# Kernel optimization log

Measured on AMD Instinct MI355X. Metric: run time of the kernel, lower is better.

## Reference

```python
import jax, jax.numpy as jnp
import numpy as np

N, D, H, C, K, L = 50000, 256, 128, 40, 4, 2
E = 800000


def setup_inputs() -> dict:
    key = jax.random.key(0)
    ks = jax.random.split(key, 20)
    g = lambda k, s: jax.random.normal(k, s, dtype=jnp.float32) * 0.05
    z = lambda s: jnp.zeros(s, dtype=jnp.float32)
    return {
        "x": jax.random.normal(ks[0], (N, D), dtype=jnp.float32),
        "edge_index": jax.random.randint(ks[1], (2, E), 0, N, dtype=jnp.int32),
        "fc0_w": g(ks[2], (D, H)), "fc0_b": z((H,)),
        "fc1_w": g(ks[3], (H, C)), "fc1_b": z((C,)),
        "env_w": g(ks[4], (L, H, K)), "env_b": z((L, K)),
        "conv_w": g(ks[5], (L, K, 2 * H, H)),
        "q_w": g(ks[6], (H, H)), "q_b": z((H,)),
        "k_w": g(ks[7], (H, H)), "k_b": z((H,)),
        "v_w": g(ks[8], (H, H)), "v_b": z((H,)),
        "envp_w": g(ks[9], (H, K)), "envp_b": z((K,)),
        "genv_w": g(ks[10], (K, H, H)),
        "gt_w": g(ks[11], (H, H)), "gt_b": z((H,)),
    }


def _gcn_conv(h, row, col, n):
    # symmetric normalization using in-degree array (deg computed from col, as in source)
    deg = jax.ops.segment_sum(jnp.ones_like(col, dtype=h.dtype), col, num_segments=n)
    inv = jnp.where(deg > 0, 1.0 / jnp.sqrt(deg), 0.0)
    val = inv[col] * inv[row]                      # [E]
    msg = val[:, None] * h[row]                    # [E, H] gather
    return jax.ops.segment_sum(msg, col, num_segments=n)  # scatter to dst


def _canet_conv(h, row, col, env, w):
    # sum_k e_k [W_D^k * A_norm h ; W_S^k * h] via cat + per-env GEMM, residual
    hi = jnp.concatenate([_gcn_conv(h, row, col, h.shape[0]), h], axis=1)  # [N, 2H]
    out_k = jnp.einsum('nd,kdh->nkh', hi, w)       # [N, K, H]
    return jnp.einsum('nk,nkh->nh', env, out_k) + h


def _linear_transformer(h, q_w, q_b, k_w, k_b, v_w, v_b, envp_w, envp_b):
    n = h.shape[0]
    q = h @ q_w + q_b
    k = h @ k_w + k_b
    v = h @ v_w + v_b
    q = q / jnp.maximum(jnp.linalg.norm(q), 1e-12)  # fro-norm of whole matrix
    k = k / jnp.maximum(jnp.linalg.norm(k), 1e-12)
    ksum = jnp.sum(k, axis=0)                       # k^T @ ones -> [H]
    attn_norm = 1.0 + (q @ ksum)[:, None] / n       # [N,1]
    gr = (v + q @ (k.T @ v) / n) / jnp.maximum(attn_norm, 1e-12)
    return gr, gr @ envp_w + envp_b


def _forward(x, edge_index, fc0_w, fc0_b, fc1_w, fc1_b, env_w, env_b, conv_w,
             q_w, q_b, k_w, k_b, v_w, v_b, envp_w, envp_b, genv_w, gt_w, gt_b):
    row, col = edge_index[0], edge_index[1]
    h = jax.nn.relu(x @ fc0_w + fc0_b)
    for i in range(L):
        logits = h @ env_w[i] + env_b[i]            # node env encoder
        env = jax.nn.softmax(logits, axis=-1)       # eval-mode sampling
        h = jax.nn.relu(_canet_conv(h, row, col, env, conv_w[i]))
    local_logits = h @ fc1_w + fc1_b                # [N, C]
    gr, glog = _linear_transformer(h, q_w, q_b, k_w, k_b, v_w, v_b, envp_w, envp_b)
    genv = jax.nn.softmax(glog, axis=-1)            # [N, K]
    gpe = jnp.einsum('nh,khe->nke', gr, genv_w)     # per-env global transforms
    ctx = jnp.einsum('nk,nkh->nh', genv, gpe)
    gh = jax.nn.relu(ctx @ gt_w + gt_b)
    global_logits = gh @ fc1_w + fc1_b
    return 0.5 * (local_logits + global_logits)     # fused prediction


def reference(x, edge_index, fc0_w, fc0_b, fc1_w, fc1_b, env_w, env_b, conv_w,
              q_w, q_b, k_w, k_b, v_w, v_b, envp_w, envp_b, genv_w, gt_w, gt_b):
    return _forward(x, edge_index, fc0_w, fc0_b, fc1_w, fc1_b, env_w, env_b, conv_w,
                    q_w, q_b, k_w, k_b, v_w, v_b, envp_w, envp_b, genv_w, gt_w, gt_b)
```

## Files before the change

### kernel.cpp

```cpp
#include <hip/hip_runtime.h>

#define DEV __device__ __forceinline__

static constexpr int NN = 50000;
static constexpr int DD = 256;
static constexpr int HH = 128;
static constexpr int CC = 40;
static constexpr int KK = 4;
static constexpr int EE = 800000;
static constexpr int MP = 50176;
static constexpr int SKV = 196;
static constexpr int CPB = 8;
static constexpr int CSB = 391;
static constexpr int MBC = 391;

typedef __attribute__((ext_vector_type(8))) short bf16x8;
typedef __attribute__((ext_vector_type(4))) float f32x4;

DEV unsigned short f2bf(float f) {
  union { float f; unsigned int i; } c; c.f = f;
  unsigned int x = c.i;
  x += 0x7FFFu + ((x >> 16) & 1u);
  return (unsigned short)(x >> 16);
}
DEV float bfbits2f(unsigned int hi16bits) {
  union { unsigned int i; float f; } c; c.i = hi16bits; return c.f;
}

__global__ void MLEI_12970801234193_kernel(float* out, int n) {
  int i = blockIdx.x * blockDim.x + threadIdx.x;
  if (i < n) out[i] = 7.0f;
}

__global__ void zero_i32_kernel(int* p, int n) {
  int i = blockIdx.x * blockDim.x + threadIdx.x;
  if (i < n) p[i] = 0;
}

__global__ void padzero_kernel(unsigned short* kT, unsigned short* vT) {
  int i = blockIdx.x * blockDim.x + threadIdx.x;
  const int PW = MP - NN;
  if (i >= HH * PW) return;
  int f = i / PW, c = i - f * PW;
  kT[(size_t)f * MP + NN + c] = 0;
  vT[(size_t)f * MP + NN + c] = 0;
}

__global__ void tcvt_kernel(const float* __restrict__ src, unsigned short* __restrict__ dst,
                            int K, int N, int nm) {
  int i = blockIdx.x * blockDim.x + threadIdx.x;
  int tot = nm * K * N;
  if (i >= tot) return;
  int m = i / (K * N);
  int rem = i - m * K * N;
  int k = rem / N;
  int n = rem - k * N;
  dst[(size_t)m * K * N + (size_t)n * K + k] = f2bf(src[i]);
}

__global__ __launch_bounds__(256) void mgemm_kernel(
    const float* __restrict__ A, const float* __restrict__ Aadd, int lda,
    const unsigned short* __restrict__ Bt, int K,
    int emode, float* __restrict__ out, int ldo,
    const float* __restrict__ bias, const float* __restrict__ resid, int ldr,
    const float* __restrict__ anorm, const float* __restrict__ red,
    unsigned short* __restrict__ outT,
    unsigned short* __restrict__ outBf, const float* __restrict__ rowscale,
    int M, int Nd) {
  __shared__ unsigned short As[2][128][40];
  __shared__ unsigned short Bs[2][128][40];
  const int tid = threadIdx.x, lane = tid & 63, wave = tid >> 6;
  const int quad = lane >> 4, l16 = lane & 15;
  const int wm = (wave >> 1) * 64, wn = (wave & 1) * 64;
  const int bm = blockIdx.x * 128;
  const int srow = tid >> 1, skh = (tid & 1) * 16;
  const int grow = bm + srow;
  const bool rowok = grow < M;
  const bool colok = srow < Nd;
  const int NCH = K >> 5;

  f32x4 acc[4][4];
#pragma unroll
  for (int i = 0; i < 4; ++i)
#pragma unroll
    for (int j = 0; j < 4; ++j)
#pragma unroll
      for (int r = 0; r < 4; ++r) acc[i][j][r] = 0.f;

  float vaA[16], vaB[16];
  bf16x8 bA0, bA1, bB0, bB1;

  auto LOAD = [&](int kc, float (&va)[16], bf16x8& b0, bf16x8& b1) {
    int k0 = kc << 5;
    if (rowok) {
      const float* ap = A + (size_t)grow * lda + k0 + skh;
      float4 v0 = *(const float4*)(ap + 0), v1 = *(const float4*)(ap + 4);
      float4 v2 = *(const float4*)(ap + 8), v3 = *(const float4*)(ap + 12);
      va[0] = v0.x; va[1] = v0.y; va[2] = v0.z; va[3] = v0.w;
      va[4] = v1.x; va[5] = v1.y; va[6] = v1.z; va[7] = v1.w;
      va[8] = v2.x; va[9] = v2.y; va[10] = v2.z; va[11] = v2.w;
      va[12] = v3.x; va[13] = v3.y; va[14] = v3.z; va[15] = v3.w;
      if (Aadd) {
        const float* ap2 = Aadd + (size_t)grow * lda + k0 + skh;
        float4 w0 = *(const float4*)(ap2 + 0), w1 = *(const float4*)(ap2 + 4);
        float4 w2 = *(const float4*)(ap2 + 8), w3 = *(const float4*)(ap2 + 12);
        va[0] += w0.x; va[1] += w0.y; va[2] += w0.z; va[3] += w0.w;
        va[4] += w1.x; va[5] += w1.y; va[6] += w1.z; va[7] += w1.w;
        va[8] += w2.x; va[9] += w2.y; va[10] += w2.z; va[11] += w2.w;
        va[12] += w3.x; va[13] += w3.y; va[14] += w3.z; va[15] += w3.w;
      }
    }
    if (colok) {
      const unsigned short* bp = Bt + (size_t)srow * K + k0 + skh;
      b0 = *(const bf16x8*)(bp);
      b1 = *(const bf16x8*)(bp + 8);
    } else {
#pragma unroll
      for (int z = 0; z < 8; ++z) { b0[z] = 0; b1[z] = 0; }
    }
  };

  auto STORE = [&](int buf, const float (&va)[16], const bf16x8& b0, const bf16x8& b1) {
    bf16x8 p0, p1;
    if (rowok) {
#pragma unroll
      for (int z = 0; z < 8; ++z) { p0[z] = (short)f2bf(va[z]); p1[z] = (short)f2bf(va[z + 8]); }
    } else {
#pragma unroll
      for (int z = 0; z < 8; ++z) { p0[z] = 0; p1[z] = 0; }
    }
    *(bf16x8*)&As[buf][srow][skh] = p0;
    *(bf16x8*)&As[buf][srow][skh + 8] = p1;
    *(bf16x8*)&Bs[buf][srow][skh] = b0;
    *(bf16x8*)&Bs[buf][srow][skh + 8] = b1;
  };

  auto MFMA = [&](int buf) {
    bf16x8 af[4], bfr[4];
#pragma unroll
    for (int i = 0; i < 4; ++i) af[i] = *(const bf16x8*)&As[buf][wm + i * 16 + l16][quad * 8];
#pragma unroll
    for (int j = 0; j < 4; ++j) bfr[j] = *(const bf16x8*)&Bs[buf][wn + j * 16 + l16][quad * 8];
#pragma unroll
    for (int i = 0; i < 4; ++i)
#pragma unroll
      for (int j = 0; j < 4; ++j)
        acc[i][j] = __builtin_amdgcn_mfma_f32_16x16x32_bf16(af[i], bfr[j], acc[i][j], 0, 0, 0);
  };

  LOAD(0, vaA, bA0, bA1);
  if (NCH > 1) LOAD(1, vaB, bB0, bB1);
  STORE(0, vaA, bA0, bA1);
  __syncthreads();

  for (int kc = 0; kc < NCH; kc += 2) {
    if (kc + 2 < NCH) LOAD(kc + 2, vaA, bA0, bA1);
    MFMA(0);
    if (kc + 1 < NCH) STORE(1, vaB, bB0, bB1);
    __syncthreads();
    if (kc + 1 < NCH) {
      if (kc + 3 < NCH) LOAD(kc + 3, vaB, bB0, bB1);
      MFMA(1);
      if (kc + 2 < NCH) STORE(0, vaA, bA0, bA1);
      __syncthreads();
    }
  }

  float s2 = (emode == 3) ? red[2] : 0.f;
#pragma unroll
  for (int j = 0; j < 4; ++j) {
    int col = wn + j * 16 + l16;
    if (col >= Nd) continue;
    float bv = bias ? bias[col] : 0.f;
#pragma unroll
    for (int i = 0; i < 4; ++i) {
      int row0 = bm + wm + i * 16 + quad * 4;
      if (row0 >= M) continue;
      float o[4];
#pragma unroll
      for (int r = 0; r < 4; ++r) {
        float a = acc[i][j][r];
        int row = row0 + r;
        if (emode == 0) o[r] = a + bv;
        else if (emode == 1) o[r] = fmaxf(a + bv, 0.f);
        else if (emode == 3) o[r] = (resid[(size_t)row * ldr + col] + a * s2) / anorm[row];
        else o[r] = 0.5f * a + bv;
        out[(size_t)row * ldo + col] = o[r];
      }
      if (outT) {
        ushort4 pk;
        pk.x = f2bf(o[0]); pk.y = f2bf(o[1]); pk.z = f2bf(o[2]); pk.w = f2bf(o[3]);
        *(ushort4*)&outT[(size_t)col * MP + row0] = pk;
      }
      if (outBf) {
#pragma unroll
        for (int r = 0; r < 4; ++r) {
          float rs = rowscale ? rowscale[row0 + r] : 1.f;
          outBf[(size_t)(row0 + r) * 128 + col] = f2bf(o[r] * rs);
        }
      }
    }
  }
}

__global__ __launch_bounds__(256) void mgemm_qkv_kernel(
    const float* __restrict__ A,
    const unsigned short* __restrict__ Btq, const unsigned short* __restrict__ Btk,
    const unsigned short* __restrict__ Btv,
    const float* __restrict__ q_b, const float* __restrict__ k_b,
    const float* __restrict__ v_b,
    float* __restrict__ outq, float* __restrict__ outk, float* __restrict__ outv,
    unsigned short* __restrict__ kT, unsigned short* __restrict__ vT, int M) {
  __shared__ unsigned short As[2][128][40];
  __shared__ unsigned short Bs[2][128][40];
  const int which = blockIdx.x % 3;
  const int bx = blockIdx.x / 3;
  const unsigned short* Bt = (which == 0) ? Btq : (which == 1) ? Btk : Btv;
  const float* bias = (which == 0) ? q_b : (which == 1) ? k_b : v_b;
  float* out = (which == 0) ? outq : (which == 1) ? outk : outv;
  unsigned short* outT = (which == 0) ? nullptr : (which == 1) ? kT : vT;

  const int tid = threadIdx.x, lane = tid & 63, wave = tid >> 6;
  const int quad = lane >> 4, l16 = lane & 15;
  const int wm = (wave >> 1) * 64, wn = (wave & 1) * 64;
  const int bm = bx * 128;
  const int srow = tid >> 1, skh = (tid & 1) * 16;
  const int grow = bm + srow;
  const bool rowok = grow < M;
  const int NCH = 4;

  f32x4 acc[4][4];
#pragma unroll
  for (int i = 0; i < 4; ++i)
#pragma unroll
    for (int j = 0; j < 4; ++j)
#pragma unroll
      for (int r = 0; r < 4; ++r) acc[i][j][r] = 0.f;

  float vaA[16], vaB[16];
  bf16x8 bA0, bA1, bB0, bB1;

  auto LOAD = [&](int kc, float (&va)[16], bf16x8& b0, bf16x8& b1) {
    int k0 = kc << 5;
    if (rowok) {
      const float* ap = A + (size_t)grow * 128 + k0 + skh;
      float4 v0 = *(const float4*)(ap + 0), v1 = *(const float4*)(ap + 4);
      float4 v2 = *(const float4*)(ap + 8), v3 = *(const float4*)(ap + 12);
      va[0] = v0.x; va[1] = v0.y; va[2] = v0.z; va[3] = v0.w;
      va[4] = v1.x; va[5] = v1.y; va[6] = v1.z; va[7] = v1.w;
      va[8] = v2.x; va[9] = v2.y; va[10] = v2.z; va[11] = v2.w;
      va[12] = v3.x; va[13] = v3.y; va[14] = v3.z; va[15] = v3.w;
    }
    const unsigned short* bp = Bt + (size_t)srow * 128 + k0 + skh;
    b0 = *(const bf16x8*)(bp);
    b1 = *(const bf16x8*)(bp + 8);
  };

  auto STORE = [&](int buf, const float (&va)[16], const bf16x8& b0, const bf16x8& b1) {
    bf16x8 p0, p1;
    if (rowok) {
#pragma unroll
      for (int z = 0; z < 8; ++z) { p0[z] = (short)f2bf(va[z]); p1[z] = (short)f2bf(va[z + 8]); }
    } else {
#pragma unroll
      for (int z = 0; z < 8; ++z) { p0[z] = 0; p1[z] = 0; }
    }
    *(bf16x8*)&As[buf][srow][skh] = p0;
    *(bf16x8*)&As[buf][srow][skh + 8] = p1;
    *(bf16x8*)&Bs[buf][srow][skh] = b0;
    *(bf16x8*)&Bs[buf][srow][skh + 8] = b1;
  };

  auto MFMA = [&](int buf) {
    bf16x8 af[4], bfr[4];
#pragma unroll
    for (int i = 0; i < 4; ++i) af[i] = *(const bf16x8*)&As[buf][wm + i * 16 + l16][quad * 8];
#pragma unroll
    for (int j = 0; j < 4; ++j) bfr[j] = *(const bf16x8*)&Bs[buf][wn + j * 16 + l16][quad * 8];
#pragma unroll
    for (int i = 0; i < 4; ++i)
#pragma unroll
      for (int j = 0; j < 4; ++j)
        acc[i][j] = __builtin_amdgcn_mfma_f32_16x16x32_bf16(af[i], bfr[j], acc[i][j], 0, 0, 0);
  };

  LOAD(0, vaA, bA0, bA1);
  LOAD(1, vaB, bB0, bB1);
  STORE(0, vaA, bA0, bA1);
  __syncthreads();

  for (int kc = 0; kc < NCH; kc += 2) {
    if (kc + 2 < NCH) LOAD(kc + 2, vaA, bA0, bA1);
    MFMA(0);
    if (kc + 1 < NCH) STORE(1, vaB, bB0, bB1);
    __syncthreads();
    if (kc + 1 < NCH) {
      if (kc + 3 < NCH) LOAD(kc + 3, vaB, bB0, bB1);
      MFMA(1);
      if (kc + 2 < NCH) STORE(0, vaA, bA0, bA1);
      __syncthreads();
    }
  }

#pragma unroll
  for (int j = 0; j < 4; ++j) {
    int col = wn + j * 16 + l16;
    float bv = bias[col];
#pragma unroll
    for (int i = 0; i < 4; ++i) {
      int row0 = bm + wm + i * 16 + quad * 4;
      if (row0 >= M) continue;
      float o[4];
#pragma unroll
      for (int r = 0; r < 4; ++r) {
        o[r] = acc[i][j][r] + bv;
        out[(size_t)(row0 + r) * 128 + col] = o[r];
      }
      if (outT) {
        ushort4 pk;
        pk.x = f2bf(o[0]); pk.y = f2bf(o[1]); pk.z = f2bf(o[2]); pk.w = f2bf(o[3]);
        *(ushort4*)&outT[(size_t)col * MP + row0] = pk;
      }
    }
  }
}

__global__ __launch_bounds__(256) void ktv_mfma_kernel(
    const unsigned short* __restrict__ kT, const unsigned short* __restrict__ vT,
    float* __restrict__ part) {
  __shared__ unsigned short As[2][128][40];
  __shared__ unsigned short Bs[2][128][40];
  const int tid = threadIdx.x, lane = tid & 63, wave = tid >> 6;
  const int quad = lane >> 4, l16 = lane & 15;
  const int wm = (wave >> 1) * 64, wn = (wave & 1) * 64;
  const int srow = tid >> 1, skh = (tid & 1) * 16;

  f32x4 acc[4][4];
#pragma unroll
  for (int i = 0; i < 4; ++i)
#pragma unroll
    for (int j = 0; j < 4; ++j)
#pragma unroll
      for (int r = 0; r < 4; ++r) acc[i][j][r] = 0.f;

  const int nb0 = blockIdx.x * (CPB * 32);
  bf16x8 kA0, kA1, vA0, vA1, kB0, kB1, vB0, vB1;

  auto LOAD = [&](int c, bf16x8& k0, bf16x8& k1, bf16x8& v0, bf16x8& v1) {
    int nb = nb0 + c * 32;
    const unsigned short* kp = kT + (size_t)srow * MP + nb + skh;
    k0 = *(const bf16x8*)(kp);
    k1 = *(const bf16x8*)(kp + 8);
    const unsigned short* vp = vT + (size_t)srow * MP + nb + skh;
    v0 = *(const bf16x8*)(vp);
    v1 = *(const bf16x8*)(vp + 8);
  };
  auto STORE = [&](int buf, const bf16x8& k0, const bf16x8& k1, const bf16x8& v0, const bf16x8& v1) {
    *(bf16x8*)&As[buf][srow][skh] = k0;
    *(bf16x8*)&As[buf][srow][skh + 8] = k1;
    *(bf16x8*)&Bs[buf][srow][skh] = v0;
    *(bf16x8*)&Bs[buf][srow][skh + 8] = v1;
  };
  auto MFMA = [&](int buf) {
    bf16x8 af[4], bfr[4];
#pragma unroll
    for (int i = 0; i < 4; ++i) af[i] = *(const bf16x8*)&As[buf][wm + i * 16 + l16][quad * 8];
#pragma unroll
    for (int j = 0; j < 4; ++j) bfr[j] = *(const bf16x8*)&Bs[buf][wn + j * 16 + l16][quad * 8];
#pragma unroll
    for (int i = 0; i < 4; ++i)
#pragma unroll
      for (int j = 0; j < 4; ++j)
        acc[i][j] = __builtin_amdgcn_mfma_f32_16x16x32_bf16(af[i], bfr[j], acc[i][j], 0, 0, 0);
  };

  LOAD(0, kA0, kA1, vA0, vA1);
  LOAD(1, kB0, kB1, vB0, vB1);
  STORE(0, kA0, kA1, vA0, vA1);
  __syncthreads();

  for (int c = 0; c < CPB; c += 2) {
    if (c + 2 < CPB) LOAD(c + 2, kA0, kA1, vA0, vA1);
    MFMA(0);
    if (c + 1 < CPB) STORE(1, kB0, kB1, vB0, vB1);
    __syncthreads();
    if (c + 1 < CPB) {
      if (c + 3 < CPB) LOAD(c + 3, kB0, kB1, vB0, vB1);
      MFMA(1);
      if (c + 2 < CPB) STORE(0, kA0, kA1, vA0, vA1);
      __syncthreads();
    }
  }

  float* pb = part + (size_t)blockIdx.x * 16384;
#pragma unroll
  for (int j = 0; j < 4; ++j) {
    int col = wn + j * 16 + l16;
#pragma unroll
    for (int i = 0; i < 4; ++i) {
      int row0 = wm + i * 16 + quad * 4;
      *(f32x4*)&pb[col * 128 + row0] = acc[i][j];
    }
  }
}

__global__ void ktv_reduce_kernel(const float* __restrict__ part,
                                  unsigned short* __restrict__ Btktv) {
  int i = blockIdx.x * blockDim.x + threadIdx.x;
  if (i >= 16384) return;
  float s0 = 0.f, s1 = 0.f, s2 = 0.f, s3 = 0.f;
  int b = 0;
  for (; b + 3 < SKV; b += 4) {
    s0 += part[(size_t)b * 16384 + i];
    s1 += part[(size_t)(b + 1) * 16384 + i];
    s2 += part[(size_t)(b + 2) * 16384 + i];
    s3 += part[(size_t)(b + 3) * 16384 + i];
  }
  for (; b < SKV; ++b) s0 += part[(size_t)b * 16384 + i];
  Btktv[i] = f2bf((s0 + s1) + (s2 + s3));
}

__global__ __launch_bounds__(256) void mconv_kernel(
    const float* __restrict__ A1, const float* __restrict__ A2,
    const float* __restrict__ env, const unsigned short* __restrict__ Btc, int Kpe,
    int relu_resid, const float* __restrict__ resid, float* __restrict__ out,
    unsigned short* __restrict__ outBf, const float* __restrict__ rowscale, int M) {
  __shared__ unsigned short As[2][128][40];
  __shared__ unsigned short Bs[2][128][40];
  const int tid = threadIdx.x, lane = tid & 63, wave = tid >> 6;
  const int quad = lane >> 4, l16 = lane & 15;
  const int wm = (wave >> 1) * 64, wn = (wave & 1) * 64;
  const int bm = blockIdx.x * 128;
  const int srow = tid >> 1, skh = (tid & 1) * 16;
  const int grow = bm + srow;
  const bool rowok = grow < M;

  float ev0 = 0.f, ev1 = 0.f, ev2 = 0.f, ev3 = 0.f;
  if (rowok) {
    float4 e4 = *(const float4*)&env[(size_t)grow * 4];
    ev0 = e4.x; ev1 = e4.y; ev2 = e4.z; ev3 = e4.w;
  }

  const int npe = Kpe >> 5;
  const int NPH = npe << 2;

  f32x4 acc[4][4];
#pragma unroll
  for (int i = 0; i < 4; ++i)
#pragma unroll
    for (int j = 0; j < 4; ++j)
#pragma unroll
      for (int r = 0; r < 4; ++r) acc[i][j][r] = 0.f;

  float aC[16], aN[16];
  bf16x8 b0, b1;

  auto LOADA = [&](int kc, float (&dst)[16]) {
    int kof = kc << 5;
    const float* Asrc = A1;
    int ks = kof;
    if (A2 && kof >= 128) { Asrc = A2; ks = kof - 128; }
    if (rowok) {
      const float* ap = Asrc + (size_t)grow * 128 + ks + skh;
      float4 v0 = *(const float4*)(ap + 0), v1 = *(const float4*)(ap + 4);
      float4 v2 = *(const float4*)(ap + 8), v3 = *(const float4*)(ap + 12);
      dst[0] = v0.x; dst[1] = v0.y; dst[2] = v0.z; dst[3] = v0.w;
      dst[4] = v1.x; dst[5] = v1.y; dst[6] = v1.z; dst[7] = v1.w;
      dst[8] = v2.x; dst[9] = v2.y; dst[10] = v2.z; dst[11] = v2.w;
      dst[12] = v3.x; dst[13] = v3.y; dst[14] = v3.z; dst[15] = v3.w;
    }
  };

  auto LOADB = [&](int e, int kc) {
    const unsigned short* bp = Btc + ((size_t)e * 128 + srow) * Kpe + (kc << 5) + skh;
    b0 = *(const bf16x8*)(bp);
    b1 = *(const bf16x8*)(bp + 8);
  };

  auto STORE = [&](int buf, const float (&a)[16], float ev) {
    bf16x8 p0, p1;
    if (rowok) {
#pragma unroll
      for (int z = 0; z < 8; ++z) {
        p0[z] = (short)f2bf(a[z] * ev);
        p1[z] = (short)f2bf(a[z + 8] * ev);
      }
    } else {
#pragma unroll
      for (int z = 0; z < 8; ++z) { p0[z] = 0; p1[z] = 0; }
    }
    *(bf16x8*)&As[buf][srow][skh] = p0;
    *(bf16x8*)&As[buf][srow][skh + 8] = p1;
    *(bf16x8*)&Bs[buf][srow][skh] = b0;
    *(bf16x8*)&Bs[buf][srow][skh + 8] = b1;
  };

  auto MFMA = [&](int buf) {
    bf16x8 af[4], bfr[4];
#pragma unroll
    for (int i = 0; i < 4; ++i) af[i] = *(const bf16x8*)&As[buf][wm + i * 16 + l16][quad * 8];
#pragma unroll
    for (int j = 0; j < 4; ++j) bfr[j] = *(const bf16x8*)&Bs[buf][wn + j * 16 + l16][quad * 8];
#pragma unroll
    for (int i = 0; i < 4; ++i)
#pragma unroll
      for (int j = 0; j < 4; ++j)
        acc[i][j] = __builtin_amdgcn_mfma_f32_16x16x32_bf16(af[i], bfr[j], acc[i][j], 0, 0, 0);
  };

  LOADA(0, aC);
  LOADB(0, 0);
  if (npe > 1) LOADA(1, aN);
  STORE(0, aC, ev0);
  __syncthreads();

  for (int kc = 0; kc < npe; ++kc) {
#pragma unroll
    for (int e = 0; e < 4; ++e) {
      const int p = (kc << 2) + e;
      const int cur = e & 1;
      const bool more = (p + 1) < NPH;
      if (more) {
        LOADB((e + 1) & 3, kc + (e == 3 ? 1 : 0));
      }
      MFMA(cur);
      if (more) {
        if (e == 3) {
#pragma unroll
          for (int z = 0; z < 16; ++z) aC[z] = aN[z];
        }
        float evn = (e == 0) ? ev1 : (e == 1) ? ev2 : (e == 2) ? ev3 : ev0;
        STORE(cur ^ 1, aC, evn);
        if (e == 3 && kc + 2 < npe) LOADA(kc + 2, aN);
      }
      __syncthreads();
    }
  }

#pragma unroll
  for (int j = 0; j < 4; ++j) {
    int col = wn + j * 16 + l16;
#pragma unroll
    for (int i = 0; i < 4; ++i) {
      int row0 = bm + wm + i * 16 + quad * 4;
      if (row0 >= M) continue;
#pragma unroll
      for (int r = 0; r < 4; ++r) {
        int row = row0 + r;
        float a = acc[i][j][r];
        float o = relu_resid ? fmaxf(a + resid[(size_t)row * 128 + col], 0.f) : a;
        out[(size_t)row * 128 + col] = o;
        if (outBf) {
          float rs = rowscale ? rowscale[row] : 1.f;
          outBf[(size_t)row * 128 + col] = f2bf(o * rs);
        }
      }
    }
  }
}

__global__ void count_kernel(const int* ei, int* deg, int E) {
  int e = blockIdx.x * blockDim.x + threadIdx.x;
  if (e >= E) return;
  atomicAdd(&deg[ei[E + e]], 1);
}

__global__ __launch_bounds__(128) void scan1_kernel(const int* __restrict__ deg,
                                                    int* __restrict__ bsum, int n) {
  __shared__ int sh[128];
  int t = threadIdx.x;
  int i = blockIdx.x * 128 + t;
  sh[t] = (i < n) ? deg[i] : 0;
  __syncthreads();
  for (int off = 64; off > 0; off >>= 1) {
    if (t < off) sh[t] += sh[t + off];
    __syncthreads();
  }
  if (t == 0) bsum[blockIdx.x] = sh[0];
}

__global__ __launch_bounds__(512) void scan2_kernel(const int* __restrict__ bsum,
                                                    int* __restrict__ boff, int nb,
                                                    int* __restrict__ startN) {
  __shared__ int sh[512];
  int t = threadIdx.x;
  int v0 = (t < nb) ? bsum[t] : 0;
  sh[t] = v0;
  __syncthreads();
  for (int off = 1; off < 512; off <<= 1) {
    int v = sh[t];
    int add = (t >= off) ? sh[t - off] : 0;
    __syncthreads();
    sh[t] = v + add;
    __syncthreads();
  }
  if (t < nb) boff[t] = sh[t] - v0;
  if (t == nb - 1) *startN = sh[t];
}

__global__ __launch_bounds__(128) void scan3_kernel(const int* __restrict__ deg,
                                                    const int* __restrict__ boff,
                                                    int* __restrict__ start,
                                                    int* __restrict__ cursor,
                                                    float* __restrict__ inv, int n) {
  __shared__ int sh[128];
  int t = threadIdx.x;
  int i = blockIdx.x * 128 + t;
  int d = (i < n) ? deg[i] : 0;
  sh[t] = d;
  __syncthreads();
  for (int off = 1; off < 128; off <<= 1) {
    int v = sh[t];
    int add = (t >= off) ? sh[t - off] : 0;
    __syncthreads();
    sh[t] = v + add;
    __syncthreads();
  }
  if (i < n) {
    int p = boff[blockIdx.x] + sh[t] - d;
    start[i] = p; cursor[i] = p;
    inv[i] = (d > 0) ? rsqrtf((float)d) : 0.f;
  }
}

__global__ void fill_kernel(const int* ei, int* cursor, int* bucket, int E) {
  int e = blockIdx.x * blockDim.x + threadIdx.x;
  if (e >= E) return;
  int r = ei[e], c = ei[E + e];
  int pos = atomicAdd(&cursor[c], 1);
  bucket[pos] = r;
}

__global__ __launch_bounds__(256) void gather_kernel(
    const unsigned short* __restrict__ hs, const int* __restrict__ start,
    const int* __restrict__ bucket, const float* __restrict__ inv,
    float* __restrict__ agg, int n) {
  int node = blockIdx.x * 4 + (threadIdx.x >> 6);
  if (node >= n) return;
  const int lane = threadIdx.x & 63;
  const int half = lane >> 5, l32 = lane & 31;
  const int f4 = l32 * 4;
  int s0 = start[node], s1 = start[node + 1];
  float a0 = 0.f, a1 = 0.f, a2 = 0.f, a3 = 0.f;
  int j = s0 + half;
  for (; j + 2 < s1; j += 4) {
    int r0 = bucket[j], r1 = bucket[j + 2];
    uint2 u0 = *(const uint2*)&hs[(size_t)r0 * 128 + f4];
    uint2 u1 = *(const uint2*)&hs[(size_t)r1 * 128 + f4];
    a0 += bfbits2f(u0.x << 16); a1 += bfbits2f(u0.x & 0xFFFF0000u);
    a2 += bfbits2f(u0.y << 16); a3 += bfbits2f(u0.y & 0xFFFF0000u);
    a0 += bfbits2f(u1.x << 16); a1 += bfbits2f(u1.x & 0xFFFF0000u);
    a2 += bfbits2f(u1.y << 16); a3 += bfbits2f(u1.y & 0xFFFF0000u);
  }
  for (; j < s1; j += 2) {
    int r = bucket[j];
    uint2 u = *(const uint2*)&hs[(size_t)r * 128 + f4];
    a0 += bfbits2f(u.x << 16); a1 += bfbits2f(u.x & 0xFFFF0000u);
    a2 += bfbits2f(u.y << 16); a3 += bfbits2f(u.y & 0xFFFF0000u);
  }
  a0 += __shfl_xor(a0, 32);
  a1 += __shfl_xor(a1, 32);
  a2 += __shfl_xor(a2, 32);
  a3 += __shfl_xor(a3, 32);
  if (half == 0) {
    float iv = inv[node];
    *(float4*)&agg[(size_t)node * 128 + f4] = make_float4(iv * a0, iv * a1, iv * a2, iv * a3);
  }
}

__global__ __launch_bounds__(256) void env_softmax_kernel(const float* __restrict__ h,
                                                          const float* __restrict__ w,
                                                          const float* __restrict__ b,
                                                          float* __restrict__ env, int M) {
  __shared__ float hsd[64][129];
  __shared__ float ws[HH * KK];
  int tid = threadIdx.x;
  int base = blockIdx.x * 64;
  for (int i = tid; i < HH * KK; i += 256) ws[i] = w[i];
  {
    int row = tid >> 2, q4 = (tid & 3) * 32;
    int g = base + row;
    if (g < M) {
      const float* hp = h + (size_t)g * HH + q4;
#pragma unroll
      for (int z = 0; z < 8; ++z) {
        float4 v = *(const float4*)(hp + z * 4);
        hsd[row][q4 + z * 4 + 0] = v.x; hsd[row][q4 + z * 4 + 1] = v.y;
        hsd[row][q4 + z * 4 + 2] = v.z; hsd[row][q4 + z * 4 + 3] = v.w;
      }
    }
  }
  __syncthreads();
  if (tid < 64 && base + tid < M) {
    float l0 = b[0], l1 = b[1], l2 = b[2], l3 = b[3];
    for (int d = 0; d < HH; ++d) {
      float hv = hsd[tid][d];
      l0 += hv * ws[d * 4 + 0]; l1 += hv * ws[d * 4 + 1];
      l2 += hv * ws[d * 4 + 2]; l3 += hv * ws[d * 4 + 3];
    }
    float m = fmaxf(fmaxf(l0, l1), fmaxf(l2, l3));
    float e0 = __expf(l0 - m), e1 = __expf(l1 - m), e2 = __expf(l2 - m), e3 = __expf(l3 - m);
    float s = 1.f / (e0 + e1 + e2 + e3);
    *(float4*)(env + (size_t)(base + tid) * KK) = make_float4(e0 * s, e1 * s, e2 * s, e3 * s);
  }
}

__global__ __launch_bounds__(256) void colstats1_kernel(
    const float* __restrict__ q, const float* __restrict__ k,
    float* __restrict__ partK, float* __restrict__ partS, int n) {
  int tid = threadIdx.x, ty = tid >> 7, tx = tid & 127;
  int lo = blockIdx.x * 128 + ty, hi = min(n, blockIdx.x * 128 + 128);
  float ks = 0.f, sq = 0.f, sk = 0.f;
  for (int r = lo; r < hi; r += 2) {
    float kv = k[(size_t)r * HH + tx];
    float qv = q[(size_t)r * HH + tx];
    ks += kv; sq += qv * qv; sk += kv * kv;
  }
  __shared__ float sks[2][128];
  __shared__ float ssq[256], ssk[256];
  sks[ty][tx] = ks; ssq[tid] = sq; ssk[tid] = sk;
  __syncthreads();
  if (ty == 0) partK[(size_t)blockIdx.x * 128 + tx] = sks[0][tx] + sks[1][tx];
  for (int off = 128; off > 0; off >>= 1) {
    if (tid < off) { ssq[tid] += ssq[tid + off]; ssk[tid] += ssk[tid + off]; }
    __syncthreads();
  }
  if (tid == 0) { partS[blockIdx.x * 2] = ssq[0]; partS[blockIdx.x * 2 + 1] = ssk[0]; }
}

__global__ __launch_bounds__(256) void colstats2_kernel(
    const float* __restrict__ partK, const float* __restrict__ partS,
    float* __restrict__ ksum, float* __restrict__ red) {
  int t = threadIdx.x;
  if (t < 128) {
    float s = 0.f;
    for (int b = 0; b < CSB; ++b) s += partK[(size_t)b * 128 + t];
    ksum[t] = s;
  } else if (t == 128 || t == 129) {
    float s = 0.f;
    for (int b = 0; b < CSB; ++b) s += partS[b * 2 + (t - 128)];
    red[t - 128] = s;
  }
}

__global__ void scale_kernel(float* red, int n) {
  float nq = fmaxf(sqrtf(red[0]), 1e-12f);
  float nk = fmaxf(sqrtf(red[1]), 1e-12f);
  red[2] = 1.f / (nq * nk * (float)n);
}

__global__ __launch_bounds__(256) void anorm_kernel(const float* q, const float* ksum,
                                                    const float* red, float* anorm, int M) {
  __shared__ float ks[HH];
  for (int i = threadIdx.x; i < HH; i += blockDim.x) ks[i] = ksum[i];
  __syncthreads();
  int n = blockIdx.x * blockDim.x + threadIdx.x;
  if (n >= M) return;
  const float* qp = q + (size_t)n * HH;
  float d = 0.f;
  for (int i = 0; i < HH; ++i) d += qp[i] * ks[i];
  float a = 1.f + d * red[2];
  anorm[n] = fmaxf(a, 1e-12f);
}

extern "C" void kernel_launch(void* const* d_in, const int* in_sizes, int n_in,
                              void* d_out, int out_size, void* d_ws, size_t ws_size,
                              hipStream_t stream) {
  const float* x = (const float*)d_in[0];
  const int* ei = (const int*)d_in[1];
  const float* fc0_w = (const float*)d_in[2];
  const float* fc0_b = (const float*)d_in[3];
  const float* fc1_w = (const float*)d_in[4];
  const float* fc1_b = (const float*)d_in[5];
  const float* env_w = (const float*)d_in[6];
  const float* env_b = (const float*)d_in[7];
  const float* conv_w = (const float*)d_in[8];
  const float* q_w = (const float*)d_in[9];
  const float* q_b = (const float*)d_in[10];
  const float* k_w = (const float*)d_in[11];
  const float* k_b = (const float*)d_in[12];
  const float* v_w = (const float*)d_in[13];
  const float* v_b = (const float*)d_in[14];
  const float* envp_w = (const float*)d_in[15];
  const float* envp_b = (const float*)d_in[16];
  const float* genv_w = (const float*)d_in[17];
  const float* gt_w = (const float*)d_in[18];
  const float* gt_b = (const float*)d_in[19];
  float* out = (float*)d_out;

  const size_t NH = (size_t)NN * HH;
  float* W = (float*)d_ws;
  float* hA = W;
  float* hB = W + NH;
  float* agg = W + 2 * NH;
  float* vbuf = W + 3 * NH;
  float* gr = W + 4 * NH;
  float* env = W + 5 * NH;
  float* genv = env + (size_t)NN * KK;
  float* inv = genv + (size_t)NN * KK;
  float* anorm = inv + NN;
  float* ksum = anorm + NN;
  float* red = ksum + HH;
  int* deg = (int*)(red + 4);
  int* start = deg + NN;
  int* cursor = start + NN + 1;
  int* bucket = cursor + NN;
  int* bsum = bucket + EE;
  int* boff = bsum + CSB;
  unsigned short* wb = (unsigned short*)(((uintptr_t)(boff + CSB) + 15) & ~(uintptr_t)15);
  unsigned short* Btfc0 = wb;
  unsigned short* Btq = Btfc0 + 32768;
  unsigned short* Btk = Btq + 16384;
  unsigned short* Btv = Btk + 16384;
  unsigned short* Btgt = Btv + 16384;
  unsigned short* Btfc1 = Btgt + 16384;
  unsigned short* Btconv = Btfc1 + 5120;
  unsigned short* Btgenv = Btconv + 262144;
  unsigned short* Btktv = Btgenv + 65536;
  unsigned short* kTbf = Btktv + 16384;
  unsigned short* vTbf = kTbf + (size_t)HH * MP;
  unsigned short* hsb = vTbf + (size_t)HH * MP;
  float* part = (float*)(((uintptr_t)(hsb + NH) + 15) & ~(uintptr_t)15);
  float* partK = part + (size_t)SKV * 16384;
  float* partS = partK + (size_t)CSB * 128;

  float* q = agg;
  float* kb = hB;
  float* ctx = hB;
  float* gh = vbuf;

  dim3 b256(256);
  const int MB = MBC;

  zero_i32_kernel<<<dim3((NN + 255) / 256), b256, 0, stream>>>(deg, NN);
  padzero_kernel<<<dim3((HH * (MP - NN) + 255) / 256), b256, 0, stream>>>(kTbf, vTbf);

  count_kernel<<<dim3((EE + 255) / 256), b256, 0, stream>>>(ei, deg, EE);
  scan1_kernel<<<dim3(CSB), dim3(128), 0, stream>>>(deg, bsum, NN);
  scan2_kernel<<<dim3(1), dim3(512), 0, stream>>>(bsum, boff, CSB, start + NN);
  scan3_kernel<<<dim3(CSB), dim3(128), 0, stream>>>(deg, boff, start, cursor, inv, NN);
  fill_kernel<<<dim3((EE + 255) / 256), b256, 0, stream>>>(ei, cursor, bucket, EE);

  tcvt_kernel<<<dim3((32768 + 255) / 256), b256, 0, stream>>>(fc0_w, Btfc0, 256, 128, 1);
  tcvt_kernel<<<dim3((16384 + 255) / 256), b256, 0, stream>>>(q_w, Btq, 128, 128, 1);
  tcvt_kernel<<<dim3((16384 + 255) / 256), b256, 0, stream>>>(k_w, Btk, 128, 128, 1);
  tcvt_kernel<<<dim3((16384 + 255) / 256), b256, 0, stream>>>(v_w, Btv, 128, 128, 1);
  tcvt_kernel<<<dim3((16384 + 255) / 256), b256, 0, stream>>>(gt_w, Btgt, 128, 128, 1);
  tcvt_kernel<<<dim3((5120 + 255) / 256), b256, 0, stream>>>(fc1_w, Btfc1, 128, 40, 1);
  tcvt_kernel<<<dim3((262144 + 255) / 256), b256, 0, stream>>>(conv_w, Btconv, 256, 128, 8);
  tcvt_kernel<<<dim3((65536 + 255) / 256), b256, 0, stream>>>(genv_w, Btgenv, 128, 128, 4);

  mgemm_kernel<<<dim3(MB), b256, 0, stream>>>(
      x, nullptr, DD, Btfc0, 256, 1, hA, HH, fc0_b, nullptr, 0, nullptr, nullptr,
      nullptr, hsb, inv, NN, HH);

  float* hcur = hA;
  float* hnext = hB;
  for (int l = 0; l < 2; ++l) {
    env_softmax_kernel<<<dim3((NN + 63) / 64), b256, 0, stream>>>(
        hcur, env_w + (size_t)l * HH * KK, env_b + (size_t)l * KK, env, NN);
    gather_kernel<<<dim3(NN / 4), b256, 0, stream>>>(hsb, start, bucket, inv, agg, NN);
    mconv_kernel<<<dim3(MB), b256, 0, stream>>>(
        agg, hcur, env, Btconv + (size_t)l * 131072, 256, 1, hcur, hnext,
        (l == 0) ? hsb : nullptr, inv, NN);
    float* t = hcur; hcur = hnext; hnext = t;
  }

  mgemm_qkv_kernel<<<dim3(3 * MB), b256, 0, stream>>>(
      hcur, Btq, Btk, Btv, q_b, k_b, v_b, q, kb, vbuf, kTbf, vTbf, NN);

  colstats1_kernel<<<dim3(CSB), b256, 0, stream>>>(q, kb, partK, partS, NN);
  colstats2_kernel<<<dim3(1), b256, 0, stream>>>(partK, partS, ksum, red);
  ktv_mfma_kernel<<<dim3(SKV), b256, 0, stream>>>(kTbf, vTbf, part);
  ktv_reduce_kernel<<<dim3(64), b256, 0, stream>>>(part, Btktv);
  scale_kernel<<<dim3(1), dim3(1), 0, stream>>>(red, NN);
  anorm_kernel<<<dim3((NN + 255) / 256), b256, 0, stream>>>(q, ksum, red, anorm, NN);

  mgemm_kernel<<<dim3(MB), b256, 0, stream>>>(
      q, nullptr, HH, Btktv, 128, 3, gr, HH, nullptr, vbuf, HH, anorm, red,
      nullptr, nullptr, nullptr, NN, HH);

  env_softmax_kernel<<<dim3((NN + 63) / 64), b256, 0, stream>>>(gr, envp_w, envp_b, genv, NN);

  mconv_kernel<<<dim3(MB), b256, 0, stream>>>(
      gr, nullptr, genv, Btgenv, 128, 0, nullptr, ctx, nullptr, nullptr, NN);

  mgemm_kernel<<<dim3(MB), b256, 0, stream>>>(
      ctx, nullptr, HH, Btgt, 128, 1, gh, HH, gt_b, nullptr, 0, nullptr, nullptr,
      nullptr, nullptr, nullptr, NN, HH);

  mgemm_kernel<<<dim3(MB), b256, 0, stream>>>(
      hcur, gh, HH, Btfc1, 128, 5, out, CC, fc1_b, nullptr, 0, nullptr, nullptr,
      nullptr, nullptr, nullptr, NN, CC);
}
```

Before: 697.9 us.

## Fuse prep kernels, merge env softmax into gather, co-launch colstats with KtV

```diff
diff --git a/kernel.cpp b/kernel.cpp
--- a/kernel.cpp
+++ b/kernel.cpp
@@ -32,30 +32,51 @@
   if (i < n) out[i] = 7.0f;
 }
 
-__global__ void zero_i32_kernel(int* p, int n) {
-  int i = blockIdx.x * blockDim.x + threadIdx.x;
-  if (i < n) p[i] = 0;
-}
-
-__global__ void padzero_kernel(unsigned short* kT, unsigned short* vT) {
-  int i = blockIdx.x * blockDim.x + threadIdx.x;
-  const int PW = MP - NN;
-  if (i >= HH * PW) return;
-  int f = i / PW, c = i - f * PW;
-  kT[(size_t)f * MP + NN + c] = 0;
-  vT[(size_t)f * MP + NN + c] = 0;
-}
-
-__global__ void tcvt_kernel(const float* __restrict__ src, unsigned short* __restrict__ dst,
-                            int K, int N, int nm) {
-  int i = blockIdx.x * blockDim.x + threadIdx.x;
-  int tot = nm * K * N;
-  if (i >= tot) return;
+DEV void tc(const float* __restrict__ src, unsigned short* __restrict__ dst,
+            int i, int K, int N) {
   int m = i / (K * N);
   int rem = i - m * K * N;
   int k = rem / N;
   int n = rem - k * N;
   dst[(size_t)m * K * N + (size_t)n * K + k] = f2bf(src[i]);
+}
+
+__global__ __launch_bounds__(256) void prep_kernel(
+    int* __restrict__ deg, unsigned short* __restrict__ kT, unsigned short* __restrict__ vT,
+    const float* __restrict__ fc0_w, unsigned short* __restrict__ Btfc0,
+    const float* __restrict__ q_w, unsigned short* __restrict__ Btq,
+    const float* __restrict__ k_w, unsigned short* __restrict__ Btk,
+    const float* __restrict__ v_w, unsigned short* __restrict__ Btv,
+    const float* __restrict__ gt_w, unsigned short* __restrict__ Btgt,
+    const float* __restrict__ fc1_w, unsigned short* __restrict__ Btfc1,
+    const float* __restrict__ conv_w, unsigned short* __restrict__ Btconv,
+    const float* __restrict__ genv_w, unsigned short* __restrict__ Btgenv) {
+  int i = blockIdx.x * 256 + threadIdx.x;
+  if (i < NN) { deg[i] = 0; return; }
+  i -= NN;
+  const int PW = MP - NN;
+  if (i < HH * PW) {
+    int f = i / PW, c = i - f * PW;
+    kT[(size_t)f * MP + NN + c] = 0;
+    vT[(size_t)f * MP + NN + c] = 0;
+    return;
+  }
+  i -= HH * PW;
+  if (i < 32768) { tc(fc0_w, Btfc0, i, 256, 128); return; }
+  i -= 32768;
+  if (i < 16384) { tc(q_w, Btq, i, 128, 128); return; }
+  i -= 16384;
+  if (i < 16384) { tc(k_w, Btk, i, 128, 128); return; }
+  i -= 16384;
+  if (i < 16384) { tc(v_w, Btv, i, 128, 128); return; }
+  i -= 16384;
+  if (i < 16384) { tc(gt_w, Btgt, i, 128, 128); return; }
+  i -= 16384;
+  if (i < 5120) { tc(fc1_w, Btfc1, i, 128, 40); return; }
+  i -= 5120;
+  if (i < 262144) { tc(conv_w, Btconv, i, 256, 128); return; }
+  i -= 262144;
+  if (i < 65536) { tc(genv_w, Btgenv, i, 128, 128); }
 }
 
 __global__ __launch_bounds__(256) void mgemm_kernel(
@@ -325,82 +346,109 @@
   }
 }
 
-__global__ __launch_bounds__(256) void ktv_mfma_kernel(
+__global__ __launch_bounds__(256) void colstats_ktv_kernel(
     const unsigned short* __restrict__ kT, const unsigned short* __restrict__ vT,
-    float* __restrict__ part) {
+    float* __restrict__ part,
+    const float* __restrict__ q, const float* __restrict__ k,
+    float* __restrict__ partK, float* __restrict__ partS, int n) {
   __shared__ unsigned short As[2][128][40];
   __shared__ unsigned short Bs[2][128][40];
-  const int tid = threadIdx.x, lane = tid & 63, wave = tid >> 6;
-  const int quad = lane >> 4, l16 = lane & 15;
-  const int wm = (wave >> 1) * 64, wn = (wave & 1) * 64;
-  const int srow = tid >> 1, skh = (tid & 1) * 16;
-
-  f32x4 acc[4][4];
-#pragma unroll
-  for (int i = 0; i < 4; ++i)
-#pragma unroll
-    for (int j = 0; j < 4; ++j)
-#pragma unroll
-      for (int r = 0; r < 4; ++r) acc[i][j][r] = 0.f;
-
-  const int nb0 = blockIdx.x * (CPB * 32);
-  bf16x8 kA0, kA1, vA0, vA1, kB0, kB1, vB0, vB1;
-
-  auto LOAD = [&](int c, bf16x8& k0, bf16x8& k1, bf16x8& v0, bf16x8& v1) {
-    int nb = nb0 + c * 32;
-    const unsigned short* kp = kT + (size_t)srow * MP + nb + skh;
-    k0 = *(const bf16x8*)(kp);
-    k1 = *(const bf16x8*)(kp + 8);
-    const unsigned short* vp = vT + (size_t)srow * MP + nb + skh;
-    v0 = *(const bf16x8*)(vp);
-    v1 = *(const bf16x8*)(vp + 8);
-  };
-  auto STORE = [&](int buf, const bf16x8& k0, const bf16x8& k1, const bf16x8& v0, const bf16x8& v1) {
-    *(bf16x8*)&As[buf][srow][skh] = k0;
-    *(bf16x8*)&As[buf][srow][skh + 8] = k1;
-    *(bf16x8*)&Bs[buf][srow][skh] = v0;
-    *(bf16x8*)&Bs[buf][srow][skh + 8] = v1;
-  };
-  auto MFMA = [&](int buf) {
-    bf16x8 af[4], bfr[4];
-#pragma unroll
-    for (int i = 0; i < 4; ++i) af[i] = *(const bf16x8*)&As[buf][wm + i * 16 + l16][quad * 8];
-#pragma unroll
-    for (int j = 0; j < 4; ++j) bfr[j] = *(const bf16x8*)&Bs[buf][wn + j * 16 + l16][quad * 8];
+  const int tid = threadIdx.x;
+
+  if (blockIdx.x < SKV) {
+    const int lane = tid & 63, wave = tid >> 6;
+    const int quad = lane >> 4, l16 = lane & 15;
+    const int wm = (wave >> 1) * 64, wn = (wave & 1) * 64;
+    const int srow = tid >> 1, skh = (tid & 1) * 16;
+
+    f32x4 acc[4][4];
 #pragma unroll
     for (int i = 0; i < 4; ++i)
 #pragma unroll
       for (int j = 0; j < 4; ++j)
-        acc[i][j] = __builtin_amdgcn_mfma_f32_16x16x32_bf16(af[i], bfr[j], acc[i][j], 0, 0, 0);
-  };
-
-  LOAD(0, kA0, kA1, vA0, vA1);
-  LOAD(1, kB0, kB1, vB0, vB1);
-  STORE(0, kA0, kA1, vA0, vA1);
-  __syncthreads();
-
-  for (int c = 0; c < CPB; c += 2) {
-    if (c + 2 < CPB) LOAD(c + 2, kA0, kA1, vA0, vA1);
-    MFMA(0);
-    if (c + 1 < CPB) STORE(1, kB0, kB1, vB0, vB1);
+#pragma unroll
+        for (int r = 0; r < 4; ++r) acc[i][j][r] = 0.f;
+
+    const int nb0 = blockIdx.x * (CPB * 32);
+    bf16x8 kA0, kA1, vA0, vA1, kB0, kB1, vB0, vB1;
+
+    auto LOAD = [&](int c, bf16x8& k0, bf16x8& k1, bf16x8& v0, bf16x8& v1) {
+      int nb = nb0 + c * 32;
+      const unsigned short* kp = kT + (size_t)srow * MP + nb + skh;
+      k0 = *(const bf16x8*)(kp);
+      k1 = *(const bf16x8*)(kp + 8);
+      const unsigned short* vp = vT + (size_t)srow * MP + nb + skh;
+      v0 = *(const bf16x8*)(vp);
+      v1 = *(const bf16x8*)(vp + 8);
+    };
+    auto STORE = [&](int buf, const bf16x8& k0, const bf16x8& k1, const bf16x8& v0, const bf16x8& v1) {
+      *(bf16x8*)&As[buf][srow][skh] = k0;
+      *(bf16x8*)&As[buf][srow][skh + 8] = k1;
+      *(bf16x8*)&Bs[buf][srow][skh] = v0;
+      *(bf16x8*)&Bs[buf][srow][skh + 8] = v1;
+    };
+    auto MFMA = [&](int buf) {
+      bf16x8 af[4], bfr[4];
+#pragma unroll
+      for (int i = 0; i < 4; ++i) af[i] = *(const bf16x8*)&As[buf][wm + i * 16 + l16][quad * 8];
+#pragma unroll
+      for (int j = 0; j < 4; ++j) bfr[j] = *(const bf16x8*)&Bs[buf][wn + j * 16 + l16][quad * 8];
+#pragma unroll
+      for (int i = 0; i < 4; ++i)
+#pragma unroll
+        for (int j = 0; j < 4; ++j)
+          acc[i][j] = __builtin_amdgcn_mfma_f32_16x16x32_bf16(af[i], bfr[j], acc[i][j], 0, 0, 0);
+    };
+
+    LOAD(0, kA0, kA1, vA0, vA1);
+    LOAD(1, kB0, kB1, vB0, vB1);
+    STORE(0, kA0, kA1, vA0, vA1);
     __syncthreads();
-    if (c + 1 < CPB) {
-      if (c + 3 < CPB) LOAD(c + 3, kB0, kB1, vB0, vB1);
-      MFMA(1);
-      if (c + 2 < CPB) STORE(0, kA0, kA1, vA0, vA1);
+
+    for (int c = 0; c < CPB; c += 2) {
+      if (c + 2 < CPB) LOAD(c + 2, kA0, kA1, vA0, vA1);
+      MFMA(0);
+      if (c + 1 < CPB) STORE(1, kB0, kB1, vB0, vB1);
       __syncthreads();
-    }
-  }
-
-  float* pb = part + (size_t)blockIdx.x * 16384;
-#pragma unroll
-  for (int j = 0; j < 4; ++j) {
-    int col = wn + j * 16 + l16;
-#pragma unroll
-    for (int i = 0; i < 4; ++i) {
-      int row0 = wm + i * 16 + quad * 4;
-      *(f32x4*)&pb[col * 128 + row0] = acc[i][j];
-    }
+      if (c + 1 < CPB) {
+        if (c + 3 < CPB) LOAD(c + 3, kB0, kB1, vB0, vB1);
+        MFMA(1);
+        if (c + 2 < CPB) STORE(0, kA0, kA1, vA0, vA1);
+        __syncthreads();
+      }
+    }
+
+    float* pb = part + (size_t)blockIdx.x * 16384;
+#pragma unroll
+    for (int j = 0; j < 4; ++j) {
+      int col = wn + j * 16 + l16;
+#pragma unroll
+      for (int i = 0; i < 4; ++i) {
+        int row0 = wm + i * 16 + quad * 4;
+        *(f32x4*)&pb[col * 128 + row0] = acc[i][j];
+      }
+    }
+  } else {
+    const int bid = blockIdx.x - SKV;
+    float* sks = (float*)&As[0][0][0];
+    float* ssq = sks + 256;
+    float* ssk = ssq + 256;
+    int ty = tid >> 7, tx = tid & 127;
+    int lo = bid * 128 + ty, hi = min(n, bid * 128 + 128);
+    float ks = 0.f, sq = 0.f, sk = 0.f;
+    for (int r = lo; r < hi; r += 2) {
+      float kv = k[(size_t)r * HH + tx];
+      float qv = q[(size_t)r * HH + tx];
+      ks += kv; sq += qv * qv; sk += kv * kv;
+    }
+    sks[ty * 128 + tx] = ks; ssq[tid] = sq; ssk[tid] = sk;
+    __syncthreads();
+    if (ty == 0) partK[(size_t)bid * 128 + tx] = sks[tx] + sks[128 + tx];
+    for (int off = 128; off > 0; off >>= 1) {
+      if (tid < off) { ssq[tid] += ssq[tid + off]; ssk[tid] += ssk[tid + off]; }
+      __syncthreads();
+    }
+    if (tid == 0) { partS[bid * 2] = ssq[0]; partS[bid * 2 + 1] = ssk[0]; }
   }
 }
 
@@ -631,15 +679,26 @@
   bucket[pos] = r;
 }
 
-__global__ __launch_bounds__(256) void gather_kernel(
+__global__ __launch_bounds__(256) void gather_env_kernel(
     const unsigned short* __restrict__ hs, const int* __restrict__ start,
     const int* __restrict__ bucket, const float* __restrict__ inv,
-    float* __restrict__ agg, int n) {
+    const float* __restrict__ h, const float* __restrict__ w,
+    const float* __restrict__ b,
+    float* __restrict__ agg, float* __restrict__ env, int n) {
   int node = blockIdx.x * 4 + (threadIdx.x >> 6);
   if (node >= n) return;
   const int lane = threadIdx.x & 63;
   const int half = lane >> 5, l32 = lane & 31;
   const int f4 = l32 * 4;
+
+  float2 hv = *(const float2*)&h[(size_t)node * 128 + 2 * lane];
+  float4 w0 = *(const float4*)&w[(size_t)(2 * lane) * 4];
+  float4 w1 = *(const float4*)&w[(size_t)(2 * lane + 1) * 4];
+  float p0 = hv.x * w0.x + hv.y * w1.x;
+  float p1 = hv.x * w0.y + hv.y * w1.y;
+  float p2 = hv.x * w0.z + hv.y * w1.z;
+  float p3 = hv.x * w0.w + hv.y * w1.w;
+
   int s0 = start[node], s1 = start[node + 1];
   float a0 = 0.f, a1 = 0.f, a2 = 0.f, a3 = 0.f;
   int j = s0 + half;
@@ -658,6 +717,15 @@
     a0 += bfbits2f(u.x << 16); a1 += bfbits2f(u.x & 0xFFFF0000u);
     a2 += bfbits2f(u.y << 16); a3 += bfbits2f(u.y & 0xFFFF0000u);
   }
+
+#pragma unroll
+  for (int s = 1; s <= 32; s <<= 1) {
+    p0 += __shfl_xor(p0, s);
+    p1 += __shfl_xor(p1, s);
+    p2 += __shfl_xor(p2, s);
+    p3 += __shfl_xor(p3, s);
+  }
+
   a0 += __shfl_xor(a0, 32);
   a1 += __shfl_xor(a1, 32);
   a2 += __shfl_xor(a2, 32);
@@ -665,6 +733,13 @@
   if (half == 0) {
     float iv = inv[node];
     *(float4*)&agg[(size_t)node * 128 + f4] = make_float4(iv * a0, iv * a1, iv * a2, iv * a3);
+  }
+  if (lane == 0) {
+    float l0 = p0 + b[0], l1 = p1 + b[1], l2 = p2 + b[2], l3 = p3 + b[3];
+    float m = fmaxf(fmaxf(l0, l1), fmaxf(l2, l3));
+    float e0 = __expf(l0 - m), e1 = __expf(l1 - m), e2 = __expf(l2 - m), e3 = __expf(l3 - m);
+    float s = 1.f / (e0 + e1 + e2 + e3);
+    *(float4*)&env[(size_t)node * 4] = make_float4(e0 * s, e1 * s, e2 * s, e3 * s);
   }
 }
 
@@ -703,29 +778,6 @@
     float s = 1.f / (e0 + e1 + e2 + e3);
     *(float4*)(env + (size_t)(base + tid) * KK) = make_float4(e0 * s, e1 * s, e2 * s, e3 * s);
   }
-}
-
-__global__ __launch_bounds__(256) void colstats1_kernel(
-    const float* __restrict__ q, const float* __restrict__ k,
-    float* __restrict__ partK, float* __restrict__ partS, int n) {
-  int tid = threadIdx.x, ty = tid >> 7, tx = tid & 127;
-  int lo = blockIdx.x * 128 + ty, hi = min(n, blockIdx.x * 128 + 128);
-  float ks = 0.f, sq = 0.f, sk = 0.f;
-  for (int r = lo; r < hi; r += 2) {
-    float kv = k[(size_t)r * HH + tx];
-    float qv = q[(size_t)r * HH + tx];
-    ks += kv; sq += qv * qv; sk += kv * kv;
-  }
-  __shared__ float sks[2][128];
-  __shared__ float ssq[256], ssk[256];
-  sks[ty][tx] = ks; ssq[tid] = sq; ssk[tid] = sk;
-  __syncthreads();
-  if (ty == 0) partK[(size_t)blockIdx.x * 128 + tx] = sks[0][tx] + sks[1][tx];
-  for (int off = 128; off > 0; off >>= 1) {
-    if (tid < off) { ssq[tid] += ssq[tid + off]; ssk[tid] += ssk[tid + off]; }
-    __syncthreads();
-  }
-  if (tid == 0) { partS[blockIdx.x * 2] = ssq[0]; partS[blockIdx.x * 2 + 1] = ssk[0]; }
 }
 
 __global__ __launch_bounds__(256) void colstats2_kernel(
@@ -831,9 +883,11 @@
 
   dim3 b256(256);
   const int MB = MBC;
-
-  zero_i32_kernel<<<dim3((NN + 255) / 256), b256, 0, stream>>>(deg, NN);
-  padzero_kernel<<<dim3((HH * (MP - NN) + 255) / 256), b256, 0, stream>>>(kTbf, vTbf);
+  const int PREP_TOT = NN + HH * (MP - NN) + 32768 + 4 * 16384 + 5120 + 262144 + 65536;
+
+  prep_kernel<<<dim3((PREP_TOT + 255) / 256), b256, 0, stream>>>(
+      deg, kTbf, vTbf, fc0_w, Btfc0, q_w, Btq, k_w, Btk, v_w, Btv,
+      gt_w, Btgt, fc1_w, Btfc1, conv_w, Btconv, genv_w, Btgenv);
 
   count_kernel<<<dim3((EE + 255) / 256), b256, 0, stream>>>(ei, deg, EE);
   scan1_kernel<<<dim3(CSB), dim3(128), 0, stream>>>(deg, bsum, NN);
@@ -841,15 +895,6 @@
   scan3_kernel<<<dim3(CSB), dim3(128), 0, stream>>>(deg, boff, start, cursor, inv, NN);
   fill_kernel<<<dim3((EE + 255) / 256), b256, 0, stream>>>(ei, cursor, bucket, EE);
 
-  tcvt_kernel<<<dim3((32768 + 255) / 256), b256, 0, stream>>>(fc0_w, Btfc0, 256, 128, 1);
-  tcvt_kernel<<<dim3((16384 + 255) / 256), b256, 0, stream>>>(q_w, Btq, 128, 128, 1);
-  tcvt_kernel<<<dim3((16384 + 255) / 256), b256, 0, stream>>>(k_w, Btk, 128, 128, 1);
-  tcvt_kernel<<<dim3((16384 + 255) / 256), b256, 0, stream>>>(v_w, Btv, 128, 128, 1);
-  tcvt_kernel<<<dim3((16384 + 255) / 256), b256, 0, stream>>>(gt_w, Btgt, 128, 128, 1);
-  tcvt_kernel<<<dim3((5120 + 255) / 256), b256, 0, stream>>>(fc1_w, Btfc1, 128, 40, 1);
-  tcvt_kernel<<<dim3((262144 + 255) / 256), b256, 0, stream>>>(conv_w, Btconv, 256, 128, 8);
-  tcvt_kernel<<<dim3((65536 + 255) / 256), b256, 0, stream>>>(genv_w, Btgenv, 128, 128, 4);
-
   mgemm_kernel<<<dim3(MB), b256, 0, stream>>>(
       x, nullptr, DD, Btfc0, 256, 1, hA, HH, fc0_b, nullptr, 0, nullptr, nullptr,
       nullptr, hsb, inv, NN, HH);
@@ -857,9 +902,9 @@
   float* hcur = hA;
   float* hnext = hB;
   for (int l = 0; l < 2; ++l) {
-    env_softmax_kernel<<<dim3((NN + 63) / 64), b256, 0, stream>>>(
-        hcur, env_w + (size_t)l * HH * KK, env_b + (size_t)l * KK, env, NN);
-    gather_kernel<<<dim3(NN / 4), b256, 0, stream>>>(hsb, start, bucket, inv, agg, NN);
+    gather_env_kernel<<<dim3(NN / 4), b256, 0, stream>>>(
+        hsb, start, bucket, inv, hcur, env_w + (size_t)l * HH * KK,
+        env_b + (size_t)l * KK, agg, env, NN);
     mconv_kernel<<<dim3(MB), b256, 0, stream>>>(
         agg, hcur, env, Btconv + (size_t)l * 131072, 256, 1, hcur, hnext,
         (l == 0) ? hsb : nullptr, inv, NN);
@@ -869,9 +914,9 @@
   mgemm_qkv_kernel<<<dim3(3 * MB), b256, 0, stream>>>(
       hcur, Btq, Btk, Btv, q_b, k_b, v_b, q, kb, vbuf, kTbf, vTbf, NN);
 
-  colstats1_kernel<<<dim3(CSB), b256, 0, stream>>>(q, kb, partK, partS, NN);
+  colstats_ktv_kernel<<<dim3(SKV + CSB), b256, 0, stream>>>(
+      kTbf, vTbf, part, q, kb, partK, partS, NN);
   colstats2_kernel<<<dim3(1), b256, 0, stream>>>(partK, partS, ksum, red);
-  ktv_mfma_kernel<<<dim3(SKV), b256, 0, stream>>>(kTbf, vTbf, part);
   ktv_reduce_kernel<<<dim3(64), b256, 0, stream>>>(part, Btktv);
   scale_kernel<<<dim3(1), dim3(1), 0, stream>>>(red, NN);
   anorm_kernel<<<dim3((NN + 255) / 256), b256, 0, stream>>>(q, ksum, red, anorm, NN);
```

New measurement: 657.3 us. 5.8% less time.
